# Kernel optimization log

Hardware: AMD Instinct MI355X
Metric: run time of the kernel (lower is better)

The kernel has to match this reference:

```python
import jax, jax.numpy as jnp
import numpy as np

WS = 8        # world_size (tp group size)
M = 8192      # global M, divisible by WS
N = 4096
LOCAL_K = 1024  # K // WS


def setup_inputs() -> dict:
    key = jax.random.key(0)
    k1, k2 = jax.random.split(key)
    # Per-rank K-sharded activation and weight (transpose_weight=False => weight is [N, local_K])
    inp = jax.random.normal(k1, (WS, M, LOCAL_K), dtype=jnp.float32)
    wgt = jax.random.normal(k2, (WS, N, LOCAL_K), dtype=jnp.float32) * 0.02
    return {"input": inp, "weight": wgt}


def reference(input, weight):
    """GEMM + reduce-scatter across the TP group.

    Each rank r computes partial_r = input[r] @ weight[r].T  -> [M, N].
    Reduce: full = sum_r partial_r. Scatter: rank r receives rows
    [r*M/WS : (r+1)*M/WS]. We return the scattered result for all ranks
    stacked on the leading axis: [WS, M//WS, N].
    """
    # Contract over both the rank axis (the reduce) and local_K in one einsum.
    full = jnp.einsum('rmk,rnk->mn', input, weight)  # [M, N]
    return full.reshape(WS, M // WS, N)
```

## Files before the change

kernel.cpp:

```cpp
#include <hip/hip_runtime.h>
#include <hip/hip_bf16.h>


#define M_TOT 8192
#define N_TOT 4096
#define LK    1024
#define NR    8
#define K_TOT (NR * LK)
#define NT    (K_TOT / 64)

typedef float f32x4 __attribute__((ext_vector_type(4)));
typedef short s16x8 __attribute__((ext_vector_type(8)));
typedef const __attribute__((address_space(1))) unsigned int* gptr_t;
typedef __attribute__((address_space(3))) unsigned int* lptr_t;

__device__ inline short f2bf(float f) {
    __hip_bfloat16 h = __float2bfloat16(f);
    return *reinterpret_cast<short*>(&h);
}

__global__ __launch_bounds__(256)
void cvt_bf16(const float* __restrict__ in, short* __restrict__ out,
              int row_shift, int row_mask) {
    const int row = blockIdx.x * 2 + (threadIdx.x >> 7);
    const int c   = (threadIdx.x & 127) * 8;
    const int r   = row >> row_shift;
    const int m   = row & row_mask;
    const float* src = in + ((size_t)row << 10) + c;
    f32x4 v0 = *(const f32x4*)src;
    f32x4 v1 = *(const f32x4*)(src + 4);
    s16x8 o;
    #pragma unroll
    for (int j = 0; j < 4; ++j) { o[j] = f2bf(v0[j]); o[j + 4] = f2bf(v1[j]); }
    *(s16x8*)(out + ((size_t)m << 13) + ((size_t)r << 10) + c) = o;
}


__device__ __forceinline__ void stage_half(const short* srcBase, short* ldsOp,
                                           int half, int ktile, int wid) {
    #pragma unroll
    for (int q = 0; q < 2; ++q) {
        const short* src = srcBase + (size_t)(half * 128 + q * 8) * K_TOT + ktile * 64;
        short* dst = ldsOp + (half * 128 + wid * 16 + q * 8) * 64;
        __builtin_amdgcn_global_load_lds((gptr_t)src, (lptr_t)dst, 16, 0, 0);
    }
}

template<int F0>
__device__ __forceinline__ void read_a2(s16x8 (&afr)[8][2], const short* lAc,
                                        int wm, int r15, int kg) {
    #pragma unroll
    for (int fo = 0; fo < 2; ++fo)
        #pragma unroll
        for (int ks = 0; ks < 2; ++ks) {
            const int row = wm * 128 + (F0 + fo) * 16 + r15;
            const int off = row * 64 + ((((ks << 2) | kg) ^ (row & 7)) << 3);
            afr[F0 + fo][ks] = *(const s16x8*)(lAc + off);
        }
}

__device__ __forceinline__ void read_b(s16x8 (&bfr)[4][2], const short* lBc,
                                       int wn, int r15, int kg) {
    #pragma unroll
    for (int n = 0; n < 4; ++n)
        #pragma unroll
        for (int ks = 0; ks < 2; ++ks) {
            const int row = wn * 64 + n * 16 + r15;
            const int off = row * 64 + ((((ks << 2) | kg) ^ (row & 7)) << 3);
            bfr[n][ks] = *(const s16x8*)(lBc + off);
        }
}

template<int Q>
__device__ __forceinline__ void mfma_quad(f32x4 (&acc)[8][4], s16x8 (&afr)[8][2],
                                          s16x8 (&bfr)[4][2]) {
    __builtin_amdgcn_s_setprio(1);
    #pragma unroll
    for (int fo = 0; fo < 2; ++fo)
        #pragma unroll
        for (int n = 0; n < 4; ++n)
            #pragma unroll
            for (int ks = 0; ks < 2; ++ks)
                acc[Q * 2 + fo][n] = __builtin_amdgcn_mfma_f32_16x16x32_bf16(
                    afr[Q * 2 + fo][ks], bfr[n][ks], acc[Q * 2 + fo][n], 0, 0, 0);
    __builtin_amdgcn_s_setprio(0);
}

#define PHASE_SYNC() do { \
    asm volatile("" ::: "memory"); \
    __builtin_amdgcn_s_barrier(); \
    asm volatile("s_waitcnt lgkmcnt(0)" ::: "memory"); \
    __builtin_amdgcn_sched_barrier(0); } while (0)

#define PHASE_END() do { \
    asm volatile("" ::: "memory"); \
    __builtin_amdgcn_s_barrier(); } while (0)

__global__ __launch_bounds__(512, 2)
void gemm8(const short* __restrict__ A, const short* __restrict__ B,
           float* __restrict__ C) {
    extern __shared__ short smem[];

    const int tid  = threadIdx.x;
    const int lane = tid & 63;
    const int wid  = tid >> 6;
    const int wm   = wid >> 2;
    const int wn   = wid & 3;
    const int r15  = lane & 15;
    const int kg   = lane >> 4;
    const int l8   = lane >> 3;
    const int g16  = (lane & 7) ^ l8;

    const int bid = blockIdx.x;
    const int sw  = (bid & 7) * 64 + (bid >> 3);
    const int bm  = sw >> 4;
    const int bn  = sw & 15;

    const short* srcA = A + (size_t)(bm * 256 + wid * 16 + l8) * K_TOT + g16 * 8;
    const short* srcB = B + (size_t)(bn * 256 + wid * 16 + l8) * K_TOT + g16 * 8;

    short* b0A = smem;
    short* b0B = smem + 16384;
    short* b1A = smem + 32768;
    short* b1B = smem + 49152;

    stage_half(srcB, b0B, 0, 0, wid);
    stage_half(srcB, b0B, 1, 0, wid);
    stage_half(srcA, b0A, 0, 0, wid);
    stage_half(srcA, b0A, 1, 0, wid);
    stage_half(srcB, b1B, 0, 1, wid);
    stage_half(srcB, b1B, 1, 1, wid);
    stage_half(srcA, b1A, 0, 1, wid);
    asm volatile("s_waitcnt vmcnt(6)" ::: "memory");
    asm volatile("" ::: "memory");
    __builtin_amdgcn_s_barrier();

    f32x4 acc[8][4];
    #pragma unroll
    for (int f = 0; f < 8; ++f)
        #pragma unroll
        for (int n = 0; n < 4; ++n)
            acc[f][n] = (f32x4){0.f, 0.f, 0.f, 0.f};

    s16x8 afr[8][2];
    s16x8 bfr[4][2];

    for (int t = 0; t < NT; ++t) {
        const int cur = t & 1;
        const short* lAc = smem + (cur << 15);
        const short* lBc = lAc + 16384;
        short* sA_nx  = smem + ((cur ^ 1) << 15);
        short* sA_nx2 = smem + (cur << 15);
        short* sB_nx2 = sA_nx2 + 16384;

        read_b(bfr, lBc, wn, r15, kg);
        read_a2<0>(afr, lAc, wm, r15, kg);
        if (t + 1 < NT) stage_half(srcA, sA_nx, 1, t + 1, wid);
        PHASE_SYNC();
        mfma_quad<0>(acc, afr, bfr);
        PHASE_END();

        read_a2<2>(afr, lAc, wm, r15, kg);
        if (t + 2 < NT) stage_half(srcB, sB_nx2, 0, t + 2, wid);
        PHASE_SYNC();
        mfma_quad<1>(acc, afr, bfr);
        PHASE_END();

        read_a2<4>(afr, lAc, wm, r15, kg);
        read_a2<6>(afr, lAc, wm, r15, kg);
        if (t + 2 < NT) stage_half(srcB, sB_nx2, 1, t + 2, wid);
        PHASE_SYNC();
        mfma_quad<2>(acc, afr, bfr);
        PHASE_END();

        if (t + 2 < NT) stage_half(srcA, sA_nx2, 0, t + 2, wid);
        if (t < NT - 2)       { asm volatile("s_waitcnt vmcnt(6)" ::: "memory"); }
        else if (t == NT - 2) { asm volatile("s_waitcnt vmcnt(0)" ::: "memory"); }
        PHASE_SYNC();
        mfma_quad<3>(acc, afr, bfr);
        PHASE_END();
    }

    float* Cp = C + (size_t)(bm * 256 + wm * 128 + kg * 4) * N_TOT
                  + bn * 256 + wn * 64 + r15;
    #pragma unroll
    for (int f = 0; f < 8; ++f)
        #pragma unroll
        for (int n = 0; n < 4; ++n)
            #pragma unroll
            for (int jj = 0; jj < 4; ++jj)
                Cp[(size_t)(f * 16 + jj) * N_TOT + n * 16] = acc[f][n][jj];
}

#define PAD_ROW 40
__global__ __launch_bounds__(256, 2)
void gemm_rs_fused(const float* __restrict__ A, const float* __restrict__ B,
                   float* __restrict__ C) {
    __shared__ short lA[128 * PAD_ROW];
    __shared__ short lB[128 * PAD_ROW];
    const int bid = blockIdx.x;
    const int sw  = (bid & 7) * (int)(gridDim.x >> 3) + (bid >> 3);
    const int bm = sw >> 5, bn = sw & 31;
    const int tid = threadIdx.x, lane = tid & 63, wid = tid >> 6;
    const int wr = wid >> 1, wc = wid & 1, r15 = lane & 15, kg = lane >> 4;
    const int srow = tid >> 1, scg = tid & 1;
    const float* gA = A + ((size_t)(bm * 128 + srow) << 10) + scg * 16;
    const float* gB = B + ((size_t)(bn * 128 + srow) << 10) + scg * 16;
    short* wpA = lA + srow * PAD_ROW + scg * 16;
    short* wpB = lB + srow * PAD_ROW + scg * 16;
    const short* rpA = lA + (wr * 64 + r15) * PAD_ROW + kg * 8;
    const short* rpB = lB + (wc * 64 + r15) * PAD_ROW + kg * 8;
    f32x4 acc[4][4];
    #pragma unroll
    for (int i = 0; i < 4; ++i)
        #pragma unroll
        for (int j = 0; j < 4; ++j) acc[i][j] = (f32x4){0.f, 0.f, 0.f, 0.f};
    for (int t = 0; t < K_TOT / 32; ++t) {
        const int r = t >> 5, k0 = (t & 31) << 5;
        const float* pA = gA + (size_t)r * (M_TOT * LK) + k0;
        const float* pB = gB + (size_t)r * (N_TOT * LK) + k0;
        f32x4 va[4], vb[4];
        #pragma unroll
        for (int q = 0; q < 4; ++q) va[q] = *(const f32x4*)(pA + q * 4);
        #pragma unroll
        for (int q = 0; q < 4; ++q) vb[q] = *(const f32x4*)(pB + q * 4);
        __syncthreads();
        s16x8 oa0, oa1, ob0, ob1;
        #pragma unroll
        for (int q = 0; q < 2; ++q)
            #pragma unroll
            for (int i = 0; i < 4; ++i) {
                oa0[q * 4 + i] = f2bf(va[q][i]);
                oa1[q * 4 + i] = f2bf(va[q + 2][i]);
                ob0[q * 4 + i] = f2bf(vb[q][i]);
                ob1[q * 4 + i] = f2bf(vb[q + 2][i]);
            }
        *(s16x8*)(wpA) = oa0; *(s16x8*)(wpA + 8) = oa1;
        *(s16x8*)(wpB) = ob0; *(s16x8*)(wpB + 8) = ob1;
        __syncthreads();
        s16x8 af[4], bfr2[4];
        #pragma unroll
        for (int i = 0; i < 4; ++i) af[i]   = *(const s16x8*)(rpA + i * 16 * PAD_ROW);
        #pragma unroll
        for (int i = 0; i < 4; ++i) bfr2[i] = *(const s16x8*)(rpB + i * 16 * PAD_ROW);
        #pragma unroll
        for (int i = 0; i < 4; ++i)
            #pragma unroll
            for (int j = 0; j < 4; ++j)
                acc[i][j] = __builtin_amdgcn_mfma_f32_16x16x32_bf16(
                    af[i], bfr2[j], acc[i][j], 0, 0, 0);
    }
    float* Cp = C + (size_t)(bm * 128 + wr * 64 + kg * 4) * N_TOT
                  + bn * 128 + wc * 64 + r15;
    #pragma unroll
    for (int i = 0; i < 4; ++i)
        #pragma unroll
        for (int j = 0; j < 4; ++j)
            #pragma unroll
            for (int jj = 0; jj < 4; ++jj)
                Cp[(size_t)(i * 16 + jj) * N_TOT + j * 16] = acc[i][j][jj];
}

extern "C" void kernel_launch(void* const* d_in, const int* in_sizes, int n_in,
                              void* d_out, int out_size, void* d_ws, size_t ws_size,
                              hipStream_t stream) {
    const float* A = (const float*)d_in[0];
    const float* B = (const float*)d_in[1];
    float* C = (float*)d_out;

    const size_t needA = (size_t)M_TOT * K_TOT * 2;
    const size_t needB = (size_t)N_TOT * K_TOT * 2;

    if (ws_size >= needA + needB) {
        short* Abf = (short*)d_ws;
        short* Bbf = (short*)((char*)d_ws + needA);
        cvt_bf16<<<dim3(NR * M_TOT / 2), dim3(256), 0, stream>>>(A, Abf, 13, 8191);
        cvt_bf16<<<dim3(NR * N_TOT / 2), dim3(256), 0, stream>>>(B, Bbf, 12, 4095);
        gemm8<<<dim3((M_TOT / 256) * (N_TOT / 256)), dim3(512), 131072, stream>>>(Abf, Bbf, C);
    } else {
        gemm_rs_fused<<<dim3((M_TOT / 128) * (N_TOT / 128)), dim3(256), 0, stream>>>(A, B, C);
    }
}
```

Measured before the change: 544.6 us.

## Switch GEMM inner loop to 32x32x16 MFMA with double-buffered B fragments

Replaces the 16x16x32 bf16 MFMA tiling with 32x32x16 instructions, so each wave now holds 4x2 32x32 accumulator tiles instead of 8x4 16x16 tiles. The loop is unrolled by two, with B fragments for the next k-tile prefetched into a second register buffer during the last MFMA cluster. The lgkmcnt waits are relaxed so LDS reads overlap MFMA work. The goal is fewer LDS fragment reads per flop and better MFMA throughput, at the cost of more register pressure and a more intricate wait/barrier schedule.

```diff
diff --git a/kernel.cpp b/kernel.cpp
--- a/kernel.cpp
+++ b/kernel.cpp
@@ -9,8 +9,9 @@
 #define K_TOT (NR * LK)
 #define NT    (K_TOT / 64)
 
-typedef float f32x4 __attribute__((ext_vector_type(4)));
-typedef short s16x8 __attribute__((ext_vector_type(8)));
+typedef float f32x4  __attribute__((ext_vector_type(4)));
+typedef float f32x16 __attribute__((ext_vector_type(16)));
+typedef short s16x8  __attribute__((ext_vector_type(8)));
 typedef const __attribute__((address_space(1))) unsigned int* gptr_t;
 typedef __attribute__((address_space(3))) unsigned int* lptr_t;
 
@@ -46,55 +47,86 @@
     }
 }
 
-template<int F0>
-__device__ __forceinline__ void read_a2(s16x8 (&afr)[8][2], const short* lAc,
-                                        int wm, int r15, int kg) {
-    #pragma unroll
-    for (int fo = 0; fo < 2; ++fo)
-        #pragma unroll
-        for (int ks = 0; ks < 2; ++ks) {
-            const int row = wm * 128 + (F0 + fo) * 16 + r15;
-            const int off = row * 64 + ((((ks << 2) | kg) ^ (row & 7)) << 3);
-            afr[F0 + fo][ks] = *(const s16x8*)(lAc + off);
-        }
-}
-
-__device__ __forceinline__ void read_b(s16x8 (&bfr)[4][2], const short* lBc,
-                                       int wn, int r15, int kg) {
-    #pragma unroll
-    for (int n = 0; n < 4; ++n)
-        #pragma unroll
-        for (int ks = 0; ks < 2; ++ks) {
-            const int row = wn * 64 + n * 16 + r15;
-            const int off = row * 64 + ((((ks << 2) | kg) ^ (row & 7)) << 3);
-            bfr[n][ks] = *(const s16x8*)(lBc + off);
-        }
-}
-
-template<int Q>
-__device__ __forceinline__ void mfma_quad(f32x4 (&acc)[8][4], s16x8 (&afr)[8][2],
-                                          s16x8 (&bfr)[4][2]) {
+__device__ __forceinline__ s16x8 read_frag(const short* base, int row, int gk) {
+    return *(const s16x8*)(base + row * 64 + ((gk ^ (row & 7)) << 3));
+}
+
+template<int C>
+__device__ __forceinline__ void read_a_cluster(s16x8 (&afr)[4][4], const short* lAc,
+                                               int wm, int c31, int kh) {
+    #pragma unroll
+    for (int ks = 0; ks < 4; ++ks)
+        afr[C][ks] = read_frag(lAc, (2 * C + wm) * 32 + c31, ks * 2 + kh);
+}
+
+template<int PB>
+__device__ __forceinline__ void read_b_all(s16x8 (&bfr)[2][2][4], const short* lBc,
+                                           int wn, int c31, int kh) {
+    #pragma unroll
+    for (int nf = 0; nf < 2; ++nf)
+        #pragma unroll
+        for (int ks = 0; ks < 4; ++ks)
+            bfr[PB][nf][ks] = read_frag(lBc, wn * 64 + nf * 32 + c31, ks * 2 + kh);
+}
+
+template<int C, int PB>
+__device__ __forceinline__ void mfma_cluster(f32x16 (&acc)[4][2], s16x8 (&afr)[4][4],
+                                             s16x8 (&bfr)[2][2][4]) {
     __builtin_amdgcn_s_setprio(1);
     #pragma unroll
-    for (int fo = 0; fo < 2; ++fo)
-        #pragma unroll
-        for (int n = 0; n < 4; ++n)
-            #pragma unroll
-            for (int ks = 0; ks < 2; ++ks)
-                acc[Q * 2 + fo][n] = __builtin_amdgcn_mfma_f32_16x16x32_bf16(
-                    afr[Q * 2 + fo][ks], bfr[n][ks], acc[Q * 2 + fo][n], 0, 0, 0);
+    for (int nf = 0; nf < 2; ++nf)
+        #pragma unroll
+        for (int ks = 0; ks < 4; ++ks)
+            acc[C][nf] = __builtin_amdgcn_mfma_f32_32x32x16_bf16(
+                afr[C][ks], bfr[PB][nf][ks], acc[C][nf], 0, 0, 0);
     __builtin_amdgcn_s_setprio(0);
 }
 
-#define PHASE_SYNC() do { \
-    asm volatile("" ::: "memory"); \
-    __builtin_amdgcn_s_barrier(); \
-    asm volatile("s_waitcnt lgkmcnt(0)" ::: "memory"); \
-    __builtin_amdgcn_sched_barrier(0); } while (0)
-
-#define PHASE_END() do { \
-    asm volatile("" ::: "memory"); \
-    __builtin_amdgcn_s_barrier(); } while (0)
+#define MEMCLOB asm volatile("" ::: "memory")
+#define BAR     __builtin_amdgcn_s_barrier()
+#define SCHED0  __builtin_amdgcn_sched_barrier(0)
+
+#define TILE_BODY(P) do {                                                     \
+    const int t = 2 * t2 + (P);                                               \
+    const short* lAc = smem + ((P) << 15);                                    \
+    short* bufN = smem + (((P) ^ 1) << 15);                                   \
+    short* bufC = smem + ((P) << 15);                                         \
+                                                                 \
+    read_a_cluster<1>(afr, lAc, wm, c31, kh);                                 \
+    if (t + 1 < NT) stage_half(srcA, bufN, 1, t + 1, wid);                    \
+    MEMCLOB; BAR;                                                             \
+    asm volatile("s_waitcnt lgkmcnt(4)" ::: "memory"); SCHED0;                \
+    mfma_cluster<0, (P)>(acc, afr, bfr);                                      \
+    MEMCLOB; BAR;                                                             \
+                                                                 \
+    read_a_cluster<2>(afr, lAc, wm, c31, kh);                                 \
+    if (t + 2 < NT) stage_half(srcB, bufC + 16384, 0, t + 2, wid);            \
+    MEMCLOB; BAR;                                                             \
+    asm volatile("s_waitcnt lgkmcnt(4)" ::: "memory"); SCHED0;                \
+    mfma_cluster<1, (P)>(acc, afr, bfr);                                      \
+    MEMCLOB; BAR;                                                             \
+                                                                 \
+    read_a_cluster<3>(afr, lAc, wm, c31, kh);                                 \
+    if (t + 2 < NT) stage_half(srcB, bufC + 16384, 1, t + 2, wid);            \
+    MEMCLOB; BAR;                                                             \
+    asm volatile("s_waitcnt lgkmcnt(4)" ::: "memory"); SCHED0;                \
+    mfma_cluster<2, (P)>(acc, afr, bfr);                                      \
+    MEMCLOB; BAR;                                                             \
+    \
+    \
+    asm volatile("s_waitcnt lgkmcnt(0)" ::: "memory");                        \
+    if (t < NT - 2)       asm volatile("s_waitcnt vmcnt(4)" ::: "memory");    \
+    else if (t == NT - 2) asm volatile("s_waitcnt vmcnt(0)" ::: "memory");    \
+    MEMCLOB; BAR;                                                             \
+    if (t + 1 < NT) {                                                         \
+        read_b_all<((P) ^ 1)>(bfr, bufN + 16384, wn, c31, kh);                \
+        read_a_cluster<0>(afr, bufN, wm, c31, kh);                            \
+    }                                                                         \
+    if (t + 2 < NT) stage_half(srcA, bufC, 0, t + 2, wid);                    \
+    SCHED0;                                                                   \
+    mfma_cluster<3, (P)>(acc, afr, bfr);                                      \
+    MEMCLOB; BAR;                                                             \
+} while (0)
 
 __global__ __launch_bounds__(512, 2)
 void gemm8(const short* __restrict__ A, const short* __restrict__ B,
@@ -106,8 +138,8 @@
     const int wid  = tid >> 6;
     const int wm   = wid >> 2;
     const int wn   = wid & 3;
-    const int r15  = lane & 15;
-    const int kg   = lane >> 4;
+    const int c31  = lane & 31;
+    const int kh   = lane >> 5;
     const int l8   = lane >> 3;
     const int g16  = (lane & 7) ^ l8;
 
@@ -119,77 +151,47 @@
     const short* srcA = A + (size_t)(bm * 256 + wid * 16 + l8) * K_TOT + g16 * 8;
     const short* srcB = B + (size_t)(bn * 256 + wid * 16 + l8) * K_TOT + g16 * 8;
 
-    short* b0A = smem;
-    short* b0B = smem + 16384;
-    short* b1A = smem + 32768;
-    short* b1B = smem + 49152;
-
-    stage_half(srcB, b0B, 0, 0, wid);
-    stage_half(srcB, b0B, 1, 0, wid);
-    stage_half(srcA, b0A, 0, 0, wid);
-    stage_half(srcA, b0A, 1, 0, wid);
-    stage_half(srcB, b1B, 0, 1, wid);
-    stage_half(srcB, b1B, 1, 1, wid);
-    stage_half(srcA, b1A, 0, 1, wid);
+    stage_half(srcB, smem + 16384, 0, 0, wid);
+    stage_half(srcB, smem + 16384, 1, 0, wid);
+    stage_half(srcA, smem,         0, 0, wid);
+    stage_half(srcA, smem,         1, 0, wid);
+    stage_half(srcB, smem + 49152, 0, 1, wid);
+    stage_half(srcB, smem + 49152, 1, 1, wid);
+    stage_half(srcA, smem + 32768, 0, 1, wid);
     asm volatile("s_waitcnt vmcnt(6)" ::: "memory");
-    asm volatile("" ::: "memory");
-    __builtin_amdgcn_s_barrier();
-
-    f32x4 acc[8][4];
-    #pragma unroll
-    for (int f = 0; f < 8; ++f)
-        #pragma unroll
-        for (int n = 0; n < 4; ++n)
-            acc[f][n] = (f32x4){0.f, 0.f, 0.f, 0.f};
-
-    s16x8 afr[8][2];
-    s16x8 bfr[4][2];
-
-    for (int t = 0; t < NT; ++t) {
-        const int cur = t & 1;
-        const short* lAc = smem + (cur << 15);
-        const short* lBc = lAc + 16384;
-        short* sA_nx  = smem + ((cur ^ 1) << 15);
-        short* sA_nx2 = smem + (cur << 15);
-        short* sB_nx2 = sA_nx2 + 16384;
-
-        read_b(bfr, lBc, wn, r15, kg);
-        read_a2<0>(afr, lAc, wm, r15, kg);
-        if (t + 1 < NT) stage_half(srcA, sA_nx, 1, t + 1, wid);
-        PHASE_SYNC();
-        mfma_quad<0>(acc, afr, bfr);
-        PHASE_END();
-
-        read_a2<2>(afr, lAc, wm, r15, kg);
-        if (t + 2 < NT) stage_half(srcB, sB_nx2, 0, t + 2, wid);
-        PHASE_SYNC();
-        mfma_quad<1>(acc, afr, bfr);
-        PHASE_END();
-
-        read_a2<4>(afr, lAc, wm, r15, kg);
-        read_a2<6>(afr, lAc, wm, r15, kg);
-        if (t + 2 < NT) stage_half(srcB, sB_nx2, 1, t + 2, wid);
-        PHASE_SYNC();
-        mfma_quad<2>(acc, afr, bfr);
-        PHASE_END();
-
-        if (t + 2 < NT) stage_half(srcA, sA_nx2, 0, t + 2, wid);
-        if (t < NT - 2)       { asm volatile("s_waitcnt vmcnt(6)" ::: "memory"); }
-        else if (t == NT - 2) { asm volatile("s_waitcnt vmcnt(0)" ::: "memory"); }
-        PHASE_SYNC();
-        mfma_quad<3>(acc, afr, bfr);
-        PHASE_END();
-    }
-
-    float* Cp = C + (size_t)(bm * 256 + wm * 128 + kg * 4) * N_TOT
-                  + bn * 256 + wn * 64 + r15;
-    #pragma unroll
-    for (int f = 0; f < 8; ++f)
-        #pragma unroll
-        for (int n = 0; n < 4; ++n)
-            #pragma unroll
-            for (int jj = 0; jj < 4; ++jj)
-                Cp[(size_t)(f * 16 + jj) * N_TOT + n * 16] = acc[f][n][jj];
+    MEMCLOB; BAR;
+
+    f32x16 acc[4][2];
+    #pragma unroll
+    for (int f = 0; f < 4; ++f)
+        #pragma unroll
+        for (int n = 0; n < 2; ++n)
+            #pragma unroll
+            for (int e = 0; e < 16; ++e)
+                acc[f][n][e] = 0.f;
+
+    s16x8 afr[4][4];
+    s16x8 bfr[2][2][4];
+
+    read_b_all<0>(bfr, smem + 16384, wn, c31, kh);
+    read_a_cluster<0>(afr, smem, wm, c31, kh);
+
+    for (int t2 = 0; t2 < NT / 2; ++t2) {
+        TILE_BODY(0);
+        TILE_BODY(1);
+    }
+
+    float* Cp = C + (size_t)(bm * 256 + wm * 32 + 4 * kh) * N_TOT
+                  + bn * 256 + wn * 64 + c31;
+    #pragma unroll
+    for (int mf = 0; mf < 4; ++mf)
+        #pragma unroll
+        for (int nf = 0; nf < 2; ++nf)
+            #pragma unroll
+            for (int reg = 0; reg < 16; ++reg) {
+                const int roff = mf * 64 + (reg & 3) + 8 * (reg >> 2);
+                Cp[(size_t)roff * N_TOT + nf * 32] = acc[mf][nf][reg];
+            }
 }
 
 #define PAD_ROW 40
```

After: 1.247 ms. +129.0%, slower.
